# Performance work log

Hardware: AMD Instinct MI355X
Metric: run time of the kernel (lower is better)

Reference implementation:

```python
import jax, jax.numpy as jnp
import numpy as np

DIM = 1024
HEADS = 16
DIM_HEAD = 64
INNER = HEADS * DIM_HEAD  # 1024
SCALE = DIM_HEAD ** -0.5


def setup_inputs() -> dict:
    key = jax.random.key(0)
    k1, k2, k3 = jax.random.split(key, 3)
    x = jax.random.normal(k1, (2, 2048, DIM), dtype=jnp.float32)
    # nn.Linear(dim, inner*3, bias=False): weight [3*inner, dim]; y = x @ W.T
    w_qkv = jax.random.normal(k2, (3 * INNER, DIM), dtype=jnp.float32) * (DIM ** -0.5)
    w_out = jax.random.normal(k3, (DIM, INNER), dtype=jnp.float32) * (INNER ** -0.5)
    return {"x": x, "w_qkv": w_qkv, "w_out": w_out}


def reference(x, w_qkv, w_out):
    b, n, _ = x.shape
    qkv = jnp.einsum('bnd,ed->bne', x, w_qkv)  # [b, n, 3*inner]
    q, k, v = jnp.split(qkv, 3, axis=-1)
    # [b, n, inner] -> [b, heads, n, dim_head]
    def to_heads(t):
        return t.reshape(b, n, HEADS, DIM_HEAD).transpose(0, 2, 1, 3)
    q, k, v = to_heads(q), to_heads(k), to_heads(v)
    dots = jnp.einsum('bhid,bhjd->bhij', q, k) * SCALE  # [b, h, n, n]
    attn = jax.nn.softmax(dots, axis=-1)
    out = jnp.einsum('bhij,bhjd->bhid', attn, v)  # [b, h, n, dim_head]
    out = out.transpose(0, 2, 1, 3).reshape(b, n, INNER)
    return jnp.einsum('bne,de->bnd', out, w_out)
```

## Files before the change

kernel.cpp:

```cpp
#include <hip/hip_runtime.h>
#include <hip/hip_bf16.h>

#define SEQ 2048
#define DIMK 1024

typedef __attribute__((ext_vector_type(8))) short bf16x8;
typedef __attribute__((ext_vector_type(4))) float f32x4;
typedef __attribute__((ext_vector_type(16))) float f32x16;

__device__ inline short f2bf(float f) {
    __hip_bfloat16 h = __float2bfloat16(f);
    return __builtin_bit_cast(short, h);
}

__device__ inline unsigned cvt_pk_bf16(float a, float b) {
    unsigned r;
    asm("v_cvt_pk_bf16_f32 %0, %1, %2" : "=v"(r) : "v"(a), "v"(b));
    return r;
}

__device__ inline unsigned shx32(unsigned v) {
    return (unsigned)__shfl_xor((int)v, 32, 64);
}

__device__ inline void gload16(const void* src, void* lds) {
    __builtin_amdgcn_global_load_lds(
        (const __attribute__((address_space(1))) unsigned int*)src,
        (__attribute__((address_space(3))) unsigned int*)lds, 16, 0, 0);
}

__global__ __launch_bounds__(256) void cast3_kernel(const float* __restrict__ x,
                                                    const float* __restrict__ wqkv,
                                                    const float* __restrict__ wout,
                                                    short* __restrict__ xb,
                                                    short* __restrict__ wqb,
                                                    short* __restrict__ wob) {
    int i = blockIdx.x * 256 + threadIdx.x;
    const float* src; short* dst; int off;
    if (i < 1048576)      { src = x;    dst = xb;  off = i; }
    else if (i < 1835008) { src = wqkv; dst = wqb; off = i - 1048576; }
    else                  { src = wout; dst = wob; off = i - 1835008; }
    float4 v = reinterpret_cast<const float4*>(src)[off];
    short4 o;
    o.x = f2bf(v.x); o.y = f2bf(v.y); o.z = f2bf(v.z); o.w = f2bf(v.w);
    reinterpret_cast<short4*>(dst)[off] = o;
}

__global__ __launch_bounds__(256) void gemm_qkv(const short* __restrict__ xb,
                                                const short* __restrict__ wb,
                                                short* __restrict__ q,
                                                short* __restrict__ k,
                                                short* __restrict__ vt) {
    __shared__ short Al[128][32];
    __shared__ short Bl[128][32];
    int tid = threadIdx.x;
    int m0 = blockIdx.x * 128;
    int n0 = blockIdx.y * 128;
    int w = tid >> 6, lane = tid & 63, lo = lane & 15, hi = lane >> 4;
    int wm = (w >> 1) * 64, wn = (w & 1) * 64;

    f32x4 acc[4][4];
    for (int a = 0; a < 4; a++)
        for (int b = 0; b < 4; b++)
            for (int r = 0; r < 4; r++) acc[a][b][r] = 0.f;

    int srow = tid >> 2, scol = (tid & 3) * 8;
    int srow1 = (tid + 256) >> 2, scol1 = ((tid + 256) & 3) * 8;

    for (int k0 = 0; k0 < DIMK; k0 += 32) {
        gload16(xb + (size_t)(m0 + srow) * DIMK + k0 + scol, (short*)Al + (w * 64) * 8);
        gload16(xb + (size_t)(m0 + srow1) * DIMK + k0 + scol1, (short*)Al + (256 + w * 64) * 8);
        gload16(wb + (size_t)(n0 + srow) * DIMK + k0 + scol, (short*)Bl + (w * 64) * 8);
        gload16(wb + (size_t)(n0 + srow1) * DIMK + k0 + scol1, (short*)Bl + (256 + w * 64) * 8);
        __syncthreads();
        bf16x8 af[4], bfr[4];
        for (int mt = 0; mt < 4; mt++)
            af[mt] = *reinterpret_cast<const bf16x8*>(&Al[wm + mt * 16 + lo][hi * 8]);
        for (int nt = 0; nt < 4; nt++)
            bfr[nt] = *reinterpret_cast<const bf16x8*>(&Bl[wn + nt * 16 + lo][hi * 8]);
        for (int mt = 0; mt < 4; mt++)
            for (int nt = 0; nt < 4; nt++)
                acc[mt][nt] = __builtin_amdgcn_mfma_f32_16x16x32_bf16(af[mt], bfr[nt],
                                                                      acc[mt][nt], 0, 0, 0);
        __syncthreads();
    }

    const float QS = 0.125f * 1.44269504088896f;
    for (int mt = 0; mt < 4; mt++) {
        int trow = m0 + wm + mt * 16 + hi * 4;
        for (int nt = 0; nt < 4; nt++) {
            int e = n0 + wn + nt * 16 + lo;
            for (int r = 0; r < 4; r++) {
                float val = acc[mt][nt][r];
                int t = trow + r;
                int b = t >> 11, nn = t & 2047;
                if (e < 1024) {
                    int h = e >> 6, dh = e & 63;
                    q[((size_t)(b * 16 + h) * SEQ + nn) * 64 + dh] = f2bf(val * QS);
                } else if (e < 2048) {
                    int e2 = e - 1024; int h = e2 >> 6, dh = e2 & 63;
                    k[((size_t)(b * 16 + h) * SEQ + nn) * 64 + dh] = f2bf(val);
                } else {
                    int e2 = e - 2048; int h = e2 >> 6, dh = e2 & 63;
                    vt[((size_t)(b * 16 + h) * 64 + dh) * SEQ + nn] = f2bf(val);
                }
            }
        }
    }
}

__global__ __launch_bounds__(256) void attn_kernel(const short* __restrict__ q,
                                                   const short* __restrict__ k,
                                                   const short* __restrict__ vt,
                                                   short* __restrict__ ao) {
    __shared__ short Kl[2][64][64];
    __shared__ short Vl[2][64][64];
    int tid = threadIdx.x;
    int w = tid >> 6, lane = tid & 63;
    int l31 = lane & 31, lh = lane >> 5;
    bool ishi = (lh != 0);
    int bh = blockIdx.y;
    int q0 = blockIdx.x * 128 + w * 32;

    const short* qb = q + (size_t)bh * SEQ * 64;
    const short* kb = k + (size_t)bh * SEQ * 64;
    const short* vb = vt + (size_t)bh * 64 * SEQ;

    bf16x8 qf[4];
    #pragma unroll
    for (int ds = 0; ds < 4; ++ds)
        qf[ds] = *reinterpret_cast<const bf16x8*>(qb + (size_t)(q0 + l31) * 64 + ds * 16 + lh * 8);

    int s0 = tid, s1 = tid + 256;
    int r0 = s0 >> 3, c0 = s0 & 7;
    int r1 = s1 >> 3, c1 = s1 & 7;
    const short* ksrc0 = kb + (size_t)r0 * 64 + ((c0 ^ (r0 & 7)) << 3);
    const short* ksrc1 = kb + (size_t)r1 * 64 + ((c1 ^ (r1 & 7)) << 3);
    const short* vsrc0 = vb + (size_t)r0 * SEQ + ((c0 ^ (r0 & 7)) << 3);
    const short* vsrc1 = vb + (size_t)r1 * SEQ + ((c1 ^ (r1 & 7)) << 3);

    float mrun = -__builtin_inff(), lrun = 0.f;
    f32x16 o0, o1;
    #pragma unroll
    for (int i = 0; i < 16; ++i) { o0[i] = 0.f; o1[i] = 0.f; }

    gload16(ksrc0, (short*)&Kl[0][0][0] + (w * 64) * 8);
    gload16(ksrc1, (short*)&Kl[0][0][0] + (256 + w * 64) * 8);
    gload16(vsrc0, (short*)&Vl[0][0][0] + (w * 64) * 8);
    gload16(vsrc1, (short*)&Vl[0][0][0] + (256 + w * 64) * 8);
    __syncthreads();

    int cur = 0;
    for (int t = 0; t < SEQ / 64; ++t) {
        if (t + 1 < SEQ / 64) {
            int kt = (t + 1) * 64;
            gload16(ksrc0 + (size_t)kt * 64, (short*)&Kl[cur ^ 1][0][0] + (w * 64) * 8);
            gload16(ksrc1 + (size_t)kt * 64, (short*)&Kl[cur ^ 1][0][0] + (256 + w * 64) * 8);
            gload16(vsrc0 + kt, (short*)&Vl[cur ^ 1][0][0] + (w * 64) * 8);
            gload16(vsrc1 + kt, (short*)&Vl[cur ^ 1][0][0] + (256 + w * 64) * 8);
        }

        #pragma unroll
        for (int kt32 = 0; kt32 < 2; ++kt32) {
            int krow = kt32 * 32 + l31;
            const short* kp = &Kl[cur][krow][0];
            f32x16 s;
            #pragma unroll
            for (int i = 0; i < 16; ++i) s[i] = 0.f;
            __builtin_amdgcn_s_setprio(1);
            #pragma unroll
            for (int ds = 0; ds < 4; ++ds) {
                bf16x8 kf = *reinterpret_cast<const bf16x8*>(
                    kp + (((ds * 2 + lh) ^ (krow & 7)) << 3));
                s = __builtin_amdgcn_mfma_f32_32x32x16_bf16(kf, qf[ds], s, 0, 0, 0);
            }
            __builtin_amdgcn_s_setprio(0);

            float pmax = s[0];
            #pragma unroll
            for (int i = 1; i < 16; ++i) pmax = fmaxf(pmax, s[i]);
            pmax = fmaxf(pmax, __shfl_xor(pmax, 32, 64));
            if (!__all(pmax - mrun <= 8.0f)) {
                float mn = fmaxf(mrun, pmax);
                float al = __builtin_exp2f(mrun - mn);
                mrun = mn; lrun *= al;
                #pragma unroll
                for (int i = 0; i < 16; ++i) { o0[i] *= al; o1[i] *= al; }
            }
            float rs = 0.f;
            #pragma unroll
            for (int i = 0; i < 16; ++i) {
                float p = __builtin_exp2f(s[i] - mrun);
                s[i] = p; rs += p;
            }
            rs += __shfl_xor(rs, 32, 64);
            lrun += rs;

            unsigned A0 = cvt_pk_bf16(s[0], s[1]),   A1 = cvt_pk_bf16(s[2], s[3]);
            unsigned B0 = cvt_pk_bf16(s[4], s[5]),   B1 = cvt_pk_bf16(s[6], s[7]);
            unsigned C0 = cvt_pk_bf16(s[8], s[9]),   C1 = cvt_pk_bf16(s[10], s[11]);
            unsigned D0 = cvt_pk_bf16(s[12], s[13]), D1 = cvt_pk_bf16(s[14], s[15]);
            unsigned E0 = ishi ? A0 : B0;
            unsigned E1 = ishi ? A1 : B1;
            unsigned F0 = ishi ? C0 : D0;
            unsigned F1 = ishi ? C1 : D1;
            unsigned pE0 = shx32(E0), pE1 = shx32(E1);
            unsigned pF0 = shx32(F0), pF1 = shx32(F1);
            int4 f0i, f1i;
            f0i.x = (int)(ishi ? pE0 : A0);
            f0i.y = (int)(ishi ? pE1 : A1);
            f0i.z = (int)(ishi ? B0 : pE0);
            f0i.w = (int)(ishi ? B1 : pE1);
            f1i.x = (int)(ishi ? pF0 : C0);
            f1i.y = (int)(ishi ? pF1 : C1);
            f1i.z = (int)(ishi ? D0 : pF0);
            f1i.w = (int)(ishi ? D1 : pF1);
            bf16x8 pf0 = __builtin_bit_cast(bf16x8, f0i);
            bf16x8 pf1 = __builtin_bit_cast(bf16x8, f1i);

            int vrow0 = l31, vrow1 = 32 + l31;
            const short* vp0 = &Vl[cur][vrow0][0];
            const short* vp1 = &Vl[cur][vrow1][0];
            __builtin_amdgcn_s_setprio(1);
            {
                int kg = kt32 * 2;
                bf16x8 v00 = *reinterpret_cast<const bf16x8*>(vp0 + (((kg * 2 + lh) ^ (vrow0 & 7)) << 3));
                o0 = __builtin_amdgcn_mfma_f32_32x32x16_bf16(v00, pf0, o0, 0, 0, 0);
                bf16x8 v10 = *reinterpret_cast<const bf16x8*>(vp1 + (((kg * 2 + lh) ^ (vrow1 & 7)) << 3));
                o1 = __builtin_amdgcn_mfma_f32_32x32x16_bf16(v10, pf0, o1, 0, 0, 0);
                kg = kt32 * 2 + 1;
                bf16x8 v01 = *reinterpret_cast<const bf16x8*>(vp0 + (((kg * 2 + lh) ^ (vrow0 & 7)) << 3));
                o0 = __builtin_amdgcn_mfma_f32_32x32x16_bf16(v01, pf1, o0, 0, 0, 0);
                bf16x8 v11 = *reinterpret_cast<const bf16x8*>(vp1 + (((kg * 2 + lh) ^ (vrow1 & 7)) << 3));
                o1 = __builtin_amdgcn_mfma_f32_32x32x16_bf16(v11, pf1, o1, 0, 0, 0);
            }
            __builtin_amdgcn_s_setprio(0);
        }

        __syncthreads();
        cur ^= 1;
    }

    float inv = 1.f / lrun;
    int b = bh >> 4, h = bh & 15;
    int qrow = q0 + l31;
    short* aop = ao + ((size_t)(b * SEQ + qrow)) * 1024 + h * 64;
    #pragma unroll
    for (int g = 0; g < 4; ++g) {
        uint2 u;
        u.x = cvt_pk_bf16(o0[4 * g] * inv, o0[4 * g + 1] * inv);
        u.y = cvt_pk_bf16(o0[4 * g + 2] * inv, o0[4 * g + 3] * inv);
        *reinterpret_cast<uint2*>(aop + 8 * g + 4 * lh) = u;
        uint2 v;
        v.x = cvt_pk_bf16(o1[4 * g] * inv, o1[4 * g + 1] * inv);
        v.y = cvt_pk_bf16(o1[4 * g + 2] * inv, o1[4 * g + 3] * inv);
        *reinterpret_cast<uint2*>(aop + 32 + 8 * g + 4 * lh) = v;
    }
}

__global__ __launch_bounds__(256) void gemm_out(const short* __restrict__ a,
                                                const short* __restrict__ b,
                                                float* __restrict__ out) {
    __shared__ short Al[128][32];
    __shared__ short Bl[128][32];
    int tid = threadIdx.x;
    int m0 = blockIdx.x * 128;
    int n0 = blockIdx.y * 128;
    int w = tid >> 6, lane = tid & 63, lo = lane & 15, hi = lane >> 4;
    int wm = (w >> 1) * 64, wn = (w & 1) * 64;

    f32x4 acc[4][4];
    for (int aa = 0; aa < 4; aa++)
        for (int bb = 0; bb < 4; bb++)
            for (int r = 0; r < 4; r++) acc[aa][bb][r] = 0.f;

    int srow = tid >> 2, scol = (tid & 3) * 8;
    int srow1 = (tid + 256) >> 2, scol1 = ((tid + 256) & 3) * 8;

    for (int k0 = 0; k0 < DIMK; k0 += 32) {
        gload16(a + (size_t)(m0 + srow) * DIMK + k0 + scol, (short*)Al + (w * 64) * 8);
        gload16(a + (size_t)(m0 + srow1) * DIMK + k0 + scol1, (short*)Al + (256 + w * 64) * 8);
        gload16(b + (size_t)(n0 + srow) * DIMK + k0 + scol, (short*)Bl + (w * 64) * 8);
        gload16(b + (size_t)(n0 + srow1) * DIMK + k0 + scol1, (short*)Bl + (256 + w * 64) * 8);
        __syncthreads();
        bf16x8 af[4], bfr[4];
        for (int mt = 0; mt < 4; mt++)
            af[mt] = *reinterpret_cast<const bf16x8*>(&Al[wm + mt * 16 + lo][hi * 8]);
        for (int nt = 0; nt < 4; nt++)
            bfr[nt] = *reinterpret_cast<const bf16x8*>(&Bl[wn + nt * 16 + lo][hi * 8]);
        for (int mt = 0; mt < 4; mt++)
            for (int nt = 0; nt < 4; nt++)
                acc[mt][nt] = __builtin_amdgcn_mfma_f32_16x16x32_bf16(af[mt], bfr[nt],
                                                                      acc[mt][nt], 0, 0, 0);
        __syncthreads();
    }

    for (int mt = 0; mt < 4; mt++) {
        int trow = m0 + wm + mt * 16 + hi * 4;
        for (int nt = 0; nt < 4; nt++) {
            int e = n0 + wn + nt * 16 + lo;
            for (int r = 0; r < 4; r++)
                out[(size_t)(trow + r) * 1024 + e] = acc[mt][nt][r];
        }
    }
}

extern "C" void kernel_launch(void* const* d_in, const int* in_sizes, int n_in,
                              void* d_out, int out_size, void* d_ws, size_t ws_size,
                              hipStream_t stream) {
    const float* x = (const float*)d_in[0];
    const float* wqkv = (const float*)d_in[1];
    const float* wout = (const float*)d_in[2];
    float* out = (float*)d_out;

    char* ws = (char*)d_ws;
    short* xb  = (short*)(ws);
    short* wqb = (short*)(ws + 8388608);
    short* wob = (short*)(ws + 8388608 + 6291456);
    short* qq  = (short*)(ws + 16777216);
    short* kk  = (short*)(ws + 25165824);
    short* vt  = (short*)(ws + 33554432);
    short* ao  = xb;

    hipLaunchKernelGGL(cast3_kernel, dim3(8192), dim3(256), 0, stream, x, wqkv, wout, xb, wqb, wob);
    hipLaunchKernelGGL(gemm_qkv, dim3(32, 24), dim3(256), 0, stream, xb, wqb, qq, kk, vt);
    hipLaunchKernelGGL(attn_kernel, dim3(16, 32), dim3(256), 0, stream, qq, kk, vt, ao);
    hipLaunchKernelGGL(gemm_out, dim3(32, 8), dim3(256), 0, stream, ao, wob, out);
}
```

Baseline: 149.5 us.

## Split attention KV sequence across two warp groups and merge in shared memory

Doubles the attention block to 512 threads, with two 4-wave groups each handling half of the key/value sequence for the same 128 queries. The partial softmax statistics and outputs are combined through shared memory at the end. This doubles the waves per block to increase latency hiding and parallelism, since the original grid has only 512 blocks. In exchange it uses much more LDS per block, which limits occupancy, and adds an epilogue with extra synchronisation.

```diff
diff --git a/kernel.cpp b/kernel.cpp
--- a/kernel.cpp
+++ b/kernel.cpp
@@ -109,29 +109,40 @@
     }
 }
 
-__global__ __launch_bounds__(256) void attn_kernel(const short* __restrict__ q,
-                                                   const short* __restrict__ k,
-                                                   const short* __restrict__ vt,
-                                                   short* __restrict__ ao) {
-    __shared__ short Kl[2][64][64];
-    __shared__ short Vl[2][64][64];
+__global__ __launch_bounds__(512, 4) void attn_kernel(const short* __restrict__ q,
+                                                      const short* __restrict__ k,
+                                                      const short* __restrict__ vt,
+                                                      short* __restrict__ ao) {
+    __shared__ __align__(16) char smem[67584];
     int tid = threadIdx.x;
     int w = tid >> 6, lane = tid & 63;
+    int g = w >> 2, wg = w & 3;
     int l31 = lane & 31, lh = lane >> 5;
     bool ishi = (lh != 0);
     int bh = blockIdx.y;
-    int q0 = blockIdx.x * 128 + w * 32;
+    int q0 = blockIdx.x * 128 + wg * 32;
 
     const short* qb = q + (size_t)bh * SEQ * 64;
-    const short* kb = k + (size_t)bh * SEQ * 64;
-    const short* vb = vt + (size_t)bh * 64 * SEQ;
+    const short* kb = k + (size_t)bh * SEQ * 64 + (size_t)(g * 1024) * 64;
+    const short* vb = vt + (size_t)bh * 64 * SEQ + g * 1024;
+
+    short* K0 = (short*)(smem + g * 16384);
+    short* K1 = (short*)(smem + g * 16384 + 8192);
+    short* V0 = (short*)(smem + 32768 + g * 16384);
+    short* V1 = (short*)(smem + 32768 + g * 16384 + 8192);
+    short* Kbuf[2] = {K0, K1};
+    short* Vbuf[2] = {V0, V1};
+    float* Obuf = (float*)smem;
+    float* Ml = (float*)(smem + 65536);
+    float* Ll = (float*)(smem + 65536 + 1024);
 
     bf16x8 qf[4];
     #pragma unroll
     for (int ds = 0; ds < 4; ++ds)
         qf[ds] = *reinterpret_cast<const bf16x8*>(qb + (size_t)(q0 + l31) * 64 + ds * 16 + lh * 8);
 
-    int s0 = tid, s1 = tid + 256;
+    int gtid = wg * 64 + lane;
+    int s0 = gtid, s1 = gtid + 256;
     int r0 = s0 >> 3, c0 = s0 & 7;
     int r1 = s1 >> 3, c1 = s1 & 7;
     const short* ksrc0 = kb + (size_t)r0 * 64 + ((c0 ^ (r0 & 7)) << 3);
@@ -144,26 +155,27 @@
     #pragma unroll
     for (int i = 0; i < 16; ++i) { o0[i] = 0.f; o1[i] = 0.f; }
 
-    gload16(ksrc0, (short*)&Kl[0][0][0] + (w * 64) * 8);
-    gload16(ksrc1, (short*)&Kl[0][0][0] + (256 + w * 64) * 8);
-    gload16(vsrc0, (short*)&Vl[0][0][0] + (w * 64) * 8);
-    gload16(vsrc1, (short*)&Vl[0][0][0] + (256 + w * 64) * 8);
+    gload16(ksrc0, Kbuf[0] + (wg * 64) * 8);
+    gload16(ksrc1, Kbuf[0] + (256 + wg * 64) * 8);
+    gload16(vsrc0, Vbuf[0] + (wg * 64) * 8);
+    gload16(vsrc1, Vbuf[0] + (256 + wg * 64) * 8);
     __syncthreads();
 
+    const int NT = 1024 / 64;
     int cur = 0;
-    for (int t = 0; t < SEQ / 64; ++t) {
-        if (t + 1 < SEQ / 64) {
+    for (int t = 0; t < NT; ++t) {
+        if (t + 1 < NT) {
             int kt = (t + 1) * 64;
-            gload16(ksrc0 + (size_t)kt * 64, (short*)&Kl[cur ^ 1][0][0] + (w * 64) * 8);
-            gload16(ksrc1 + (size_t)kt * 64, (short*)&Kl[cur ^ 1][0][0] + (256 + w * 64) * 8);
-            gload16(vsrc0 + kt, (short*)&Vl[cur ^ 1][0][0] + (w * 64) * 8);
-            gload16(vsrc1 + kt, (short*)&Vl[cur ^ 1][0][0] + (256 + w * 64) * 8);
+            gload16(ksrc0 + (size_t)kt * 64, Kbuf[cur ^ 1] + (wg * 64) * 8);
+            gload16(ksrc1 + (size_t)kt * 64, Kbuf[cur ^ 1] + (256 + wg * 64) * 8);
+            gload16(vsrc0 + kt, Vbuf[cur ^ 1] + (wg * 64) * 8);
+            gload16(vsrc1 + kt, Vbuf[cur ^ 1] + (256 + wg * 64) * 8);
         }
 
         #pragma unroll
         for (int kt32 = 0; kt32 < 2; ++kt32) {
             int krow = kt32 * 32 + l31;
-            const short* kp = &Kl[cur][krow][0];
+            const short* kp = Kbuf[cur] + krow * 64;
             f32x16 s;
             #pragma unroll
             for (int i = 0; i < 16; ++i) s[i] = 0.f;
@@ -219,8 +231,8 @@
             bf16x8 pf1 = __builtin_bit_cast(bf16x8, f1i);
 
             int vrow0 = l31, vrow1 = 32 + l31;
-            const short* vp0 = &Vl[cur][vrow0][0];
-            const short* vp1 = &Vl[cur][vrow1][0];
+            const short* vp0 = Vbuf[cur] + vrow0 * 64;
+            const short* vp1 = Vbuf[cur] + vrow1 * 64;
             __builtin_amdgcn_s_setprio(1);
             {
                 int kg = kt32 * 2;
@@ -241,20 +253,50 @@
         cur ^= 1;
     }
 
-    float inv = 1.f / lrun;
-    int b = bh >> 4, h = bh & 15;
-    int qrow = q0 + l31;
-    short* aop = ao + ((size_t)(b * SEQ + qrow)) * 1024 + h * 64;
-    #pragma unroll
-    for (int g = 0; g < 4; ++g) {
-        uint2 u;
-        u.x = cvt_pk_bf16(o0[4 * g] * inv, o0[4 * g + 1] * inv);
-        u.y = cvt_pk_bf16(o0[4 * g + 2] * inv, o0[4 * g + 3] * inv);
-        *reinterpret_cast<uint2*>(aop + 8 * g + 4 * lh) = u;
-        uint2 v;
-        v.x = cvt_pk_bf16(o1[4 * g] * inv, o1[4 * g + 1] * inv);
-        v.y = cvt_pk_bf16(o1[4 * g + 2] * inv, o1[4 * g + 3] * inv);
-        *reinterpret_cast<uint2*>(aop + 32 + 8 * g + 4 * lh) = v;
+    int qloc = wg * 32 + l31;
+    Ml[g * 128 + qloc] = mrun;
+    Ll[g * 128 + qloc] = lrun;
+    __syncthreads();
+    float mo = Ml[(1 - g) * 128 + qloc];
+    float lo2 = Ll[(1 - g) * 128 + qloc];
+    float mtot = fmaxf(mrun, mo);
+    float wself = __builtin_exp2f(mrun - mtot);
+    float woth = __builtin_exp2f(mo - mtot);
+    float ltot = wself * lrun + woth * lo2;
+
+    if (g == 1) {
+        #pragma unroll
+        for (int i = 0; i < 16; ++i) {
+            int d0 = (i & 3) + 8 * (i >> 2) + 4 * lh;
+            Obuf[qloc * 65 + d0]      = wself * o0[i];
+            Obuf[qloc * 65 + 32 + d0] = wself * o1[i];
+        }
+    }
+    __syncthreads();
+    if (g == 0) {
+        float inv = 1.f / ltot;
+        int b = bh >> 4, h = bh & 15;
+        int qrow = q0 + l31;
+        short* aop = ao + ((size_t)(b * SEQ + qrow)) * 1024 + h * 64;
+        #pragma unroll
+        for (int gg = 0; gg < 4; ++gg) {
+            float v0 = (wself * o0[4 * gg + 0] + Obuf[qloc * 65 + (0 + 8 * gg + 4 * lh)]) * inv;
+            float v1 = (wself * o0[4 * gg + 1] + Obuf[qloc * 65 + (1 + 8 * gg + 4 * lh)]) * inv;
+            float v2 = (wself * o0[4 * gg + 2] + Obuf[qloc * 65 + (2 + 8 * gg + 4 * lh)]) * inv;
+            float v3 = (wself * o0[4 * gg + 3] + Obuf[qloc * 65 + (3 + 8 * gg + 4 * lh)]) * inv;
+            uint2 u;
+            u.x = cvt_pk_bf16(v0, v1);
+            u.y = cvt_pk_bf16(v2, v3);
+            *reinterpret_cast<uint2*>(aop + 8 * gg + 4 * lh) = u;
+            float y0 = (wself * o1[4 * gg + 0] + Obuf[qloc * 65 + 32 + (0 + 8 * gg + 4 * lh)]) * inv;
+            float y1 = (wself * o1[4 * gg + 1] + Obuf[qloc * 65 + 32 + (1 + 8 * gg + 4 * lh)]) * inv;
+            float y2 = (wself * o1[4 * gg + 2] + Obuf[qloc * 65 + 32 + (2 + 8 * gg + 4 * lh)]) * inv;
+            float y3 = (wself * o1[4 * gg + 3] + Obuf[qloc * 65 + 32 + (3 + 8 * gg + 4 * lh)]) * inv;
+            uint2 u2;
+            u2.x = cvt_pk_bf16(y0, y1);
+            u2.y = cvt_pk_bf16(y2, y3);
+            *reinterpret_cast<uint2*>(aop + 32 + 8 * gg + 4 * lh) = u2;
+        }
     }
 }
 
@@ -324,6 +366,6 @@
 
     hipLaunchKernelGGL(cast3_kernel, dim3(8192), dim3(256), 0, stream, x, wqkv, wout, xb, wqb, wob);
     hipLaunchKernelGGL(gemm_qkv, dim3(32, 24), dim3(256), 0, stream, xb, wqb, qq, kk, vt);
-    hipLaunchKernelGGL(attn_kernel, dim3(16, 32), dim3(256), 0, stream, qq, kk, vt, ao);
+    hipLaunchKernelGGL(attn_kernel, dim3(16, 32), dim3(512), 0, stream, qq, kk, vt, ao);
     hipLaunchKernelGGL(gemm_out, dim3(32, 8), dim3(256), 0, stream, ao, wob, out);
 }
```

Result: faster. 141.7 us (-5.2%).
